# Kernel tuning notes

Hardware: AMD Instinct MI355X
Metric: run time of the kernel (lower is better)

The kernel has to match this reference:

```python
import jax, jax.numpy as jnp
import numpy as np

B, D, S, SE, H, DFF = 4, 1024, 1024, 1024, 16, 4096
DH = D // H
NUDGE = 1e-7


def norm(x):
    # x: [B, D, S]; custom layer norm: mean over (1,2), then divide by full L2 norm
    size = x.shape[1] * x.shape[2]
    mean = jnp.sum(x, axis=(1, 2)) / size
    x = x - mean[:, None, None]
    std = jnp.sqrt(jnp.sum(x * x, axis=(1, 2)))
    return x / (std[:, None, None] + NUDGE)


def mha(q_in, kv_in, Wq, Wk, Wv, Wo, causal):
    # q_in: [B, Sq, D], kv_in: [B, Sk, D]
    Bq, Sq, _ = q_in.shape
    Sk = kv_in.shape[1]
    q = (q_in @ Wq).reshape(Bq, Sq, H, DH)
    k = (kv_in @ Wk).reshape(Bq, Sk, H, DH)
    v = (kv_in @ Wv).reshape(Bq, Sk, H, DH)
    scores = jnp.einsum('bqhd,bkhd->bhqk', q, k) / jnp.sqrt(jnp.asarray(DH, q.dtype))
    if causal:
        mask = jnp.tril(jnp.ones((Sq, Sk), dtype=bool))
        scores = jnp.where(mask, scores, jnp.finfo(scores.dtype).min)
    attn = jax.nn.softmax(scores, axis=-1)
    out = jnp.einsum('bhqk,bkhd->bqhd', attn, v).reshape(Bq, Sq, D)
    return out @ Wo


def setup_inputs() -> dict:
    key = jax.random.key(0)
    ks = jax.random.split(key, 13)
    w = lambda k, sh: jax.random.normal(k, sh, dtype=jnp.float32) * 0.02
    return {
        'embedding': jax.random.normal(ks[0], (B, D, SE), dtype=jnp.float32),
        'other_inputs': jax.random.normal(ks[1], (B, D, S), dtype=jnp.float32),
        'Wq_s': w(ks[2], (D, D)), 'Wk_s': w(ks[3], (D, D)),
        'Wv_s': w(ks[4], (D, D)), 'Wo_s': w(ks[5], (D, D)),
        'Wq_c': w(ks[6], (D, D)), 'Wk_c': w(ks[7], (D, D)),
        'Wv_c': w(ks[8], (D, D)), 'Wo_c': w(ks[9], (D, D)),
        'W1': w(ks[10], (D, DFF)), 'b1': jnp.zeros((DFF,), jnp.float32),
        'W2': w(ks[11], (DFF, D)), 'b2': jnp.zeros((D,), jnp.float32),
    }


def reference(embedding, other_inputs, Wq_s, Wk_s, Wv_s, Wo_s,
              Wq_c, Wk_c, Wv_c, Wo_c, W1, b1, W2, b2):
    # tensors are [B, D, S]; attention operates on [B, S, D]
    x = other_inputs.transpose(0, 2, 1)
    sa = mha(x, x, Wq_s, Wk_s, Wv_s, Wo_s, causal=True)
    post_attention = norm(other_inputs + sa.transpose(0, 2, 1))

    pa = post_attention.transpose(0, 2, 1)
    emb = embedding.transpose(0, 2, 1)
    ca = mha(pa, emb, Wq_c, Wk_c, Wv_c, Wo_c, causal=False)
    post_embedding = norm(post_attention + ca.transpose(0, 2, 1))

    # per-token MLP (original loops over axis 2 and restacks; here fully batched)
    pe = post_embedding.transpose(0, 2, 1)  # [B, S, D]
    ff = jax.nn.relu(pe @ W1 + b1) @ W2 + b2
    return norm(post_embedding + ff.transpose(0, 2, 1))
```

## Files before the change

### kernel.cpp

```cpp
#include <hip/hip_runtime.h>
#include <cmath>

#define B_   4
#define D_   1024
#define S_   1024
#define H_   16
#define DH_  64
#define DFF_ 4096

typedef __attribute__((ext_vector_type(8))) short bf16x8;
typedef __attribute__((ext_vector_type(4))) float f32x4;

__device__ __forceinline__ unsigned short f2b(float f) {
    unsigned int u = __float_as_uint(f);
    u += 0x7fffu + ((u >> 16) & 1u);
    return (unsigned short)(u >> 16);
}

__device__ __forceinline__ void gload_lds16(const unsigned short* g, unsigned short* l) {
    __builtin_amdgcn_global_load_lds(
        (const __attribute__((address_space(1))) void*)g,
        (__attribute__((address_space(3))) void*)l, 16, 0, 0);
}

template <int BM, int BN, bool RES>
__global__ __launch_bounds__(256, 2)
void gemm_t(const unsigned short* __restrict__ A,
            const unsigned short* __restrict__ Wt,
            const float* __restrict__ bias,
            const float* __restrict__ residual,
            float* __restrict__ Cf, unsigned short* __restrict__ Cb,
            float* __restrict__ partial,
            int N, int K, int lda, int ldb, long csplit, int relu)
{
    constexpr int FM = BM / 32, FN = BN / 32;
    __shared__ unsigned short As[BM * 32];
    __shared__ unsigned short Bs[BN * 32];
    const int tid = threadIdx.x;
    const int w = tid >> 6, lane = tid & 63;
    const int quad = lane >> 4, l16 = lane & 15;
    const int m0 = blockIdx.x * BM, n0 = blockIdx.y * BN;
    const int wm = (w >> 1) * (BM / 2), wn = (w & 1) * (BN / 2);
    const int srow = lane >> 2, scol = (lane & 3) * 8;

    A  += (size_t)blockIdx.z * K;
    Wt += (size_t)blockIdx.z * K;
    if (Cf) Cf += (size_t)blockIdx.z * csplit;

    f32x4 acc[FM][FN] = {};

    for (int k0 = 0; k0 < K; k0 += 32) {
#pragma unroll
        for (int i = 0; i < BM / 64; ++i)
            gload_lds16(A + (size_t)(m0 + (w + 4 * i) * 16 + srow) * lda + k0 + scol,
                        As + (w + 4 * i) * 512);
#pragma unroll
        for (int i = 0; i < BN / 64; ++i)
            gload_lds16(Wt + (size_t)(n0 + (w + 4 * i) * 16 + srow) * ldb + k0 + scol,
                        Bs + (w + 4 * i) * 512);
        __syncthreads();

        bf16x8 af[FM], bfr[FN];
#pragma unroll
        for (int i = 0; i < FM; ++i)
            af[i] = *(const bf16x8*)&As[(wm + i * 16 + l16) * 32 + quad * 8];
#pragma unroll
        for (int j = 0; j < FN; ++j)
            bfr[j] = *(const bf16x8*)&Bs[(wn + j * 16 + l16) * 32 + quad * 8];
#pragma unroll
        for (int i = 0; i < FM; ++i)
#pragma unroll
            for (int j = 0; j < FN; ++j)
                acc[i][j] = __builtin_amdgcn_mfma_f32_16x16x32_bf16(af[i], bfr[j], acc[i][j], 0, 0, 0);
        __syncthreads();
    }

    float s = 0.f, ss = 0.f;
#pragma unroll
    for (int i = 0; i < FM; ++i) {
        const int grow = m0 + wm + i * 16 + quad * 4;
#pragma unroll
        for (int j = 0; j < FN; ++j) {
            const int gcol = n0 + wn + j * 16 + l16;
            const float bv = bias ? bias[gcol] : 0.f;
#pragma unroll
            for (int r = 0; r < 4; ++r) {
                float vv = acc[i][j][r] + bv;
                if (relu) vv = fmaxf(vv, 0.f);
                if constexpr (RES) {
                    vv += residual[(size_t)(grow + r) * N + gcol];
                    s += vv; ss += vv * vv;
                    Cf[(size_t)(grow + r) * N + gcol] = vv;
                } else {
                    if (Cf) Cf[(size_t)(grow + r) * N + gcol] = vv;
                    if (Cb) Cb[(size_t)(grow + r) * N + gcol] = f2b(vv);
                }
            }
        }
    }

    if constexpr (RES) {
        float* rs = (float*)As;
        float* rss = rs + 256;
        rs[tid] = s; rss[tid] = ss;
        __syncthreads();
        for (int off = 128; off > 0; off >>= 1) {
            if (tid < off) { rs[tid] += rs[tid + off]; rss[tid] += rss[tid + off]; }
            __syncthreads();
        }
        if (tid == 0) {
            constexpr int YPB = S_ / BM;
            const int b = blockIdx.x / YPB;
            const int chunk = (blockIdx.x % YPB) * gridDim.y + blockIdx.y;
            const int chunks = YPB * gridDim.y;
            partial[((size_t)b * chunks + chunk) * 2 + 0] = rs[0];
            partial[((size_t)b * chunks + chunk) * 2 + 1] = rss[0];
        }
    }
}

__global__ void reduce2_res(const float* __restrict__ pc, const float* __restrict__ res,
                            const float* __restrict__ bias, float* __restrict__ y,
                            float* __restrict__ partial)
{
    const size_t pcs = (size_t)4096 * 1024;
    const int b = blockIdx.y;
    const size_t base = (size_t)b * 1048576 + (size_t)blockIdx.x * 16384;
    float s = 0.f, ss = 0.f;
    for (int i = threadIdx.x; i < 4096; i += 256) {
        const size_t e = base + (size_t)i * 4;
        float4 v0 = *(const float4*)&pc[e];
        float4 v1 = *(const float4*)&pc[e + pcs];
        float4 rv = *(const float4*)&res[e];
        float4 bv = *(const float4*)&bias[e & 1023];
        float4 o;
        o.x = v0.x + v1.x + rv.x + bv.x;
        o.y = v0.y + v1.y + rv.y + bv.y;
        o.z = v0.z + v1.z + rv.z + bv.z;
        o.w = v0.w + v1.w + rv.w + bv.w;
        *(float4*)&y[e] = o;
        s += o.x + o.y + o.z + o.w;
        ss += o.x * o.x + o.y * o.y + o.z * o.z + o.w * o.w;
    }
    __shared__ float rs[256], rss[256];
    rs[threadIdx.x] = s; rss[threadIdx.x] = ss;
    __syncthreads();
    for (int off = 128; off > 0; off >>= 1) {
        if (threadIdx.x < off) {
            rs[threadIdx.x] += rs[threadIdx.x + off];
            rss[threadIdx.x] += rss[threadIdx.x + off];
        }
        __syncthreads();
    }
    if (threadIdx.x == 0) {
        partial[((size_t)b * 64 + blockIdx.x) * 2 + 0] = rs[0];
        partial[((size_t)b * 64 + blockIdx.x) * 2 + 1] = rss[0];
    }
}

__device__ __forceinline__ void stats_reduce(const float* __restrict__ partial,
                                             int b, int chunks, int tid,
                                             float* rs, float* rss,
                                             float& mean, float& inv)
{
    float s = 0.f, ss = 0.f;
    for (int i = tid; i < chunks; i += 256) {
        s  += partial[((size_t)b * chunks + i) * 2 + 0];
        ss += partial[((size_t)b * chunks + i) * 2 + 1];
    }
    rs[tid] = s; rss[tid] = ss;
    __syncthreads();
    for (int off = 128; off > 0; off >>= 1) {
        if (tid < off) { rs[tid] += rs[tid + off]; rss[tid] += rss[tid + off]; }
        __syncthreads();
    }
    const float size = (float)(D_ * S_);
    const float m = rs[0] / size;
    const float var = fmaxf(rss[0] - size * m * m, 0.f);
    mean = m;
    inv = 1.f / (sqrtf(var) + 1e-7f);
    __syncthreads();
}

__global__ void norm_apply_dual(float* __restrict__ y, unsigned short* __restrict__ yb,
                                const float* __restrict__ partial, int chunks)
{
    __shared__ float rs[256], rss[256];
    const int b = blockIdx.y;
    float mean, inv;
    stats_reduce(partial, b, chunks, threadIdx.x, rs, rss, mean, inv);

    const int perBatch = D_ * S_;
    float4* y4 = (float4*)(y + (size_t)b * perBatch);
    unsigned short* yb_ = yb + (size_t)b * perBatch;
    const int n4 = perBatch / 4;
    for (int i = blockIdx.x * blockDim.x + threadIdx.x; i < n4;
         i += gridDim.x * blockDim.x) {
        float4 v = y4[i];
        v.x = (v.x - mean) * inv; v.y = (v.y - mean) * inv;
        v.z = (v.z - mean) * inv; v.w = (v.w - mean) * inv;
        y4[i] = v;
        ushort4 hh; hh.x = f2b(v.x); hh.y = f2b(v.y); hh.z = f2b(v.z); hh.w = f2b(v.w);
        *(ushort4*)(yb_ + (size_t)i * 4) = hh;
    }
}

template <bool CAUSAL>
__global__ __launch_bounds__(256, 2)
void attn_mfma2(const unsigned short* __restrict__ q, const unsigned short* __restrict__ k,
                const unsigned short* __restrict__ vt, unsigned short* __restrict__ o,
                int qstride, int kstride)
{
    __shared__ unsigned short Ks[64][72];
    __shared__ unsigned short Vt[64][72];
    __shared__ unsigned short Ps[4][2][16][72];
    const int tid = threadIdx.x;
    const int w = tid >> 6, lane = tid & 63;
    const int quad = lane >> 4, l16 = lane & 15;
    const int h = blockIdx.y, b = blockIdx.z;
    const int qt = CAUSAL ? ((blockIdx.x + h) & 7) : blockIdx.x;
    const int q0 = qt * 128;

    const unsigned short* qA = q + (size_t)(b * S_ + q0 + w * 16 + l16) * qstride + h * DH_;
    const unsigned short* qB = qA + (size_t)64 * qstride;
    const bf16x8 qa0 = *(const bf16x8*)(qA + quad * 8);
    const bf16x8 qa1 = *(const bf16x8*)(qA + 32 + quad * 8);
    const bf16x8 qb0 = *(const bf16x8*)(qB + quad * 8);
    const bf16x8 qb1 = *(const bf16x8*)(qB + 32 + quad * 8);

    f32x4 OA[4] = {}, OB[4] = {};
    float lA[4] = {}, lB[4] = {};

    const int nblk = CAUSAL ? (2 * qt + 2) : (S_ / 64);
    for (int t = 0; t < nblk; ++t) {
        const int j0 = t * 64;
#pragma unroll
        for (int it = 0; it < 2; ++it) {
            const int id2 = tid + it * 256;
            const int row = id2 >> 3, c8 = (id2 & 7) * 8;
            *(bf16x8*)&Ks[row][c8] =
                *(const bf16x8*)(k + (size_t)(b * S_ + j0 + row) * kstride + h * DH_ + c8);
            *(bf16x8*)&Vt[row][c8] =
                *(const bf16x8*)(vt + (size_t)((b * H_ + h) * DH_ + row) * S_ + j0 + c8);
        }
        __syncthreads();

        const bool doA = !CAUSAL || (t <= 2 * qt);
        const bool diagA = CAUSAL && (t == 2 * qt);
        const bool diagB = CAUSAL && (t == 2 * qt + 1);

        f32x4 stA[4], stB[4];
#pragma unroll
        for (int n = 0; n < 4; ++n) {
            const bf16x8 kf0 = *(const bf16x8*)&Ks[n * 16 + l16][quad * 8];
            const bf16x8 kf1 = *(const bf16x8*)&Ks[n * 16 + l16][32 + quad * 8];
            if (doA) {
                f32x4 c = {};
                c = __builtin_amdgcn_mfma_f32_16x16x32_bf16(qa0, kf0, c, 0, 0, 0);
                c = __builtin_amdgcn_mfma_f32_16x16x32_bf16(qa1, kf1, c, 0, 0, 0);
                stA[n] = c;
            }
            f32x4 c = {};
            c = __builtin_amdgcn_mfma_f32_16x16x32_bf16(qb0, kf0, c, 0, 0, 0);
            c = __builtin_amdgcn_mfma_f32_16x16x32_bf16(qb1, kf1, c, 0, 0, 0);
            stB[n] = c;
        }

        if (doA) {
#pragma unroll
            for (int n = 0; n < 4; ++n)
#pragma unroll
                for (int r = 0; r < 4; ++r) {
                    float sv = stA[n][r] * 0.125f;
                    if (diagA) {
                        const int row = q0 + w * 16 + quad * 4 + r;
                        const int key = j0 + n * 16 + l16;
                        if (key > row) sv = -1e30f;
                    }
                    const float p = __expf(sv);
                    lA[r] += p;
                    Ps[w][0][quad * 4 + r][n * 16 + l16] = f2b(p);
                }
        }
#pragma unroll
        for (int n = 0; n < 4; ++n)
#pragma unroll
            for (int r = 0; r < 4; ++r) {
                float sv = stB[n][r] * 0.125f;
                if (diagB) {
                    const int row = q0 + 64 + w * 16 + quad * 4 + r;
                    const int key = j0 + n * 16 + l16;
                    if (key > row) sv = -1e30f;
                }
                const float p = __expf(sv);
                lB[r] += p;
                Ps[w][1][quad * 4 + r][n * 16 + l16] = f2b(p);
            }
        __threadfence_block();

        const bf16x8 pa0 = *(const bf16x8*)&Ps[w][0][l16][quad * 8];
        const bf16x8 pa1 = *(const bf16x8*)&Ps[w][0][l16][32 + quad * 8];
        const bf16x8 pb0 = *(const bf16x8*)&Ps[w][1][l16][quad * 8];
        const bf16x8 pb1 = *(const bf16x8*)&Ps[w][1][l16][32 + quad * 8];
#pragma unroll
        for (int n = 0; n < 4; ++n) {
            const bf16x8 vf0 = *(const bf16x8*)&Vt[n * 16 + l16][quad * 8];
            const bf16x8 vf1 = *(const bf16x8*)&Vt[n * 16 + l16][32 + quad * 8];
            if (doA) {
                OA[n] = __builtin_amdgcn_mfma_f32_16x16x32_bf16(pa0, vf0, OA[n], 0, 0, 0);
                OA[n] = __builtin_amdgcn_mfma_f32_16x16x32_bf16(pa1, vf1, OA[n], 0, 0, 0);
            }
            OB[n] = __builtin_amdgcn_mfma_f32_16x16x32_bf16(pb0, vf0, OB[n], 0, 0, 0);
            OB[n] = __builtin_amdgcn_mfma_f32_16x16x32_bf16(pb1, vf1, OB[n], 0, 0, 0);
        }
        __syncthreads();
    }

#pragma unroll
    for (int r = 0; r < 4; ++r) {
        float la = lA[r], lb = lB[r];
        la += __shfl_xor(la, 1); la += __shfl_xor(la, 2);
        la += __shfl_xor(la, 4); la += __shfl_xor(la, 8);
        lb += __shfl_xor(lb, 1); lb += __shfl_xor(lb, 2);
        lb += __shfl_xor(lb, 4); lb += __shfl_xor(lb, 8);
        const float ia = 1.f / la, ib = 1.f / lb;
        const size_t baseA = (size_t)(b * S_ + q0 + w * 16 + quad * 4 + r) * D_ + h * DH_;
        const size_t baseB = baseA + (size_t)64 * D_;
#pragma unroll
        for (int n = 0; n < 4; ++n) {
            o[baseA + n * 16 + l16] = f2b(OA[n][r] * ia);
            o[baseB + n * 16 + l16] = f2b(OB[n][r] * ib);
        }
    }
}

__global__ void transpose_v(const unsigned short* __restrict__ src,
                            unsigned short* __restrict__ dst, int istride)
{
    __shared__ unsigned short t[32][34];
    const int z = blockIdx.z, b = z >> 4, h = z & 15;
    const int s0 = blockIdx.x * 32, d0 = blockIdx.y * 32;
    const int tx = threadIdx.x, ty = threadIdx.y;
#pragma unroll
    for (int i = 0; i < 4; ++i)
        t[ty + i * 8][tx] =
            src[(size_t)(b * S_ + s0 + ty + i * 8) * istride + h * DH_ + d0 + tx];
    __syncthreads();
#pragma unroll
    for (int i = 0; i < 4; ++i)
        dst[(size_t)(z * DH_ + d0 + ty + i * 8) * S_ + s0 + tx] = t[tx][ty + i * 8];
}

struct SrcPack { const float* p[8]; };

__global__ void wtrans8(SrcPack pk, unsigned short* __restrict__ dst)
{
    __shared__ float tile[32][33];
    const int z = blockIdx.z;
    const float* src = pk.p[z];
    const int c0 = blockIdx.x * 32, r0 = blockIdx.y * 32;
    const int tx = threadIdx.x, ty = threadIdx.y;
#pragma unroll
    for (int i = 0; i < 4; ++i)
        tile[ty + i * 8][tx] = src[(size_t)(r0 + ty + i * 8) * 1024 + c0 + tx];
    __syncthreads();
#pragma unroll
    for (int i = 0; i < 4; ++i)
        dst[(size_t)z * 1048576 + (size_t)(c0 + ty + i * 8) * 1024 + r0 + tx] =
            f2b(tile[tx][ty + i * 8]);
}

__global__ void transpose_dual(const float* __restrict__ in, float* __restrict__ outf,
                               unsigned short* __restrict__ outb, int R, int C,
                               const float* __restrict__ partial, int chunks)
{
    __shared__ float tile[32][33];
    __shared__ float rs[256], rss[256];
    const int z = blockIdx.z;
    const int tx = threadIdx.x, ty = threadIdx.y;
    const int tid = ty * 32 + tx;

    float mean = 0.f, inv = 1.f;
    if (partial) {
        float s = 0.f, ss = 0.f;
        for (int i = tid; i < chunks; i += 256) {
            s  += partial[((size_t)z * chunks + i) * 2 + 0];
            ss += partial[((size_t)z * chunks + i) * 2 + 1];
        }
        rs[tid] = s; rss[tid] = ss;
        __syncthreads();
        for (int off = 128; off > 0; off >>= 1) {
            if (tid < off) { rs[tid] += rs[tid + off]; rss[tid] += rss[tid + off]; }
            __syncthreads();
        }
        const float size = (float)(D_ * S_);
        mean = rs[0] / size;
        const float var = fmaxf(rss[0] - size * mean * mean, 0.f);
        inv = 1.f / (sqrtf(var) + 1e-7f);
        __syncthreads();
    }

    const float* ip = in + (size_t)z * R * C;
    const int c0 = blockIdx.x * 32, r0 = blockIdx.y * 32;
#pragma unroll
    for (int i = 0; i < 4; ++i)
        tile[ty + i * 8][tx] = ip[(size_t)(r0 + ty + i * 8) * C + c0 + tx];
    __syncthreads();
#pragma unroll
    for (int i = 0; i < 4; ++i) {
        const float v = (tile[tx][ty + i * 8] - mean) * inv;
        const size_t oidx = (size_t)z * R * C + (size_t)(c0 + ty + i * 8) * R + r0 + tx;
        if (outf) outf[oidx] = v;
        if (outb) outb[oidx] = f2b(v);
    }
}

extern "C" void kernel_launch(void* const* d_in, const int* in_sizes, int n_in,
                              void* d_out, int out_size, void* d_ws, size_t ws_size,
                              hipStream_t stream)
{
    const float* embedding = (const float*)d_in[0];
    const float* other     = (const float*)d_in[1];
    const float* W1 = (const float*)d_in[10];
    const float* b1 = (const float*)d_in[11];
    const float* W2 = (const float*)d_in[12];
    const float* b2 = (const float*)d_in[13];
    float* out = (float*)d_out;

    char* wsb = (char*)d_ws;
    const size_t MB = 1u << 20;
    float* f0 = (float*)(wsb + 0 * MB);
    float* f2 = (float*)(wsb + 16 * MB);
    unsigned short* wts  = (unsigned short*)(wsb + 32 * MB);
    unsigned short* wqkv = wts;
    unsigned short* wo_s = wts + 3 * 1048576;
    unsigned short* wq_c = wts + 4 * 1048576;
    unsigned short* wkv_c= wts + 5 * 1048576;
    unsigned short* wo_c = wts + 7 * 1048576;
    unsigned short* w1t  = wts + 8 * 1048576;
    unsigned short* w2t  = wts + 12 * 1048576;
    unsigned short* actA = (unsigned short*)(wsb + 64 * MB);
    unsigned short* actB = (unsigned short*)(wsb + 72 * MB);
    unsigned short* actC = (unsigned short*)(wsb + 80 * MB);
    unsigned short* actC2 = actC + 4 * 1048576;
    float* pc      = (float*)(wsb + 112 * MB);
    float* partial = (float*)(wsb + 176 * MB);

    const dim3 blkT(32, 8), blk256(256);
    const dim3 gT(32, 32, B_);
    const dim3 gAttn(S_ / 128, H_, B_);
    const dim3 gVt(32, 2, B_ * H_);
    const dim3 gApply(64, B_);

    SrcPack pk;
    pk.p[0] = (const float*)d_in[2]; pk.p[1] = (const float*)d_in[3];
    pk.p[2] = (const float*)d_in[4]; pk.p[3] = (const float*)d_in[5];
    pk.p[4] = (const float*)d_in[6]; pk.p[5] = (const float*)d_in[7];
    pk.p[6] = (const float*)d_in[8]; pk.p[7] = (const float*)d_in[9];
    hipLaunchKernelGGL(wtrans8, dim3(32, 32, 8), blkT, 0, stream, pk, wts);
    hipLaunchKernelGGL(transpose_dual, dim3(128, 32, 1), blkT, 0, stream, W1, nullptr, w1t, 1024, 4096, nullptr, 0);
    hipLaunchKernelGGL(transpose_dual, dim3(32, 128, 1), blkT, 0, stream, W2, nullptr, w2t, 4096, 1024, nullptr, 0);

    hipLaunchKernelGGL(transpose_dual, gT, blkT, 0, stream, other, f0, actA, D_, S_, nullptr, 0);

    hipLaunchKernelGGL((gemm_t<128, 128, false>), dim3(32, 24), blk256, 0, stream,
                       actA, wqkv, nullptr, nullptr, nullptr, actC, nullptr,
                       3072, 1024, 1024, 1024, 0L, 0);
    hipLaunchKernelGGL(transpose_v, gVt, blkT, 0, stream, actC + 2048, actA, 3072);
    hipLaunchKernelGGL(attn_mfma2<true>, gAttn, blk256, 0, stream,
                       actC, actC + 1024, actA, actB, 3072, 3072);
    hipLaunchKernelGGL((gemm_t<64, 128, true>), dim3(64, 8), blk256, 0, stream,
                       actB, wo_s, nullptr, f0, f2, nullptr, partial,
                       1024, 1024, 1024, 1024, 0L, 0);
    hipLaunchKernelGGL(norm_apply_dual, gApply, blk256, 0, stream, f2, actA, partial, 128);

    hipLaunchKernelGGL(transpose_dual, gT, blkT, 0, stream, embedding, nullptr, actB, D_, S_, nullptr, 0);
    hipLaunchKernelGGL((gemm_t<64, 128, false>), dim3(64, 8), blk256, 0, stream,
                       actA, wq_c, nullptr, nullptr, nullptr, actC, nullptr,
                       1024, 1024, 1024, 1024, 0L, 0);
    hipLaunchKernelGGL((gemm_t<128, 128, false>), dim3(32, 16), blk256, 0, stream,
                       actB, wkv_c, nullptr, nullptr, nullptr, actC2, nullptr,
                       2048, 1024, 1024, 1024, 0L, 0);
    hipLaunchKernelGGL(transpose_v, gVt, blkT, 0, stream, actC2 + 1024, actB, 2048);
    hipLaunchKernelGGL(attn_mfma2<false>, gAttn, blk256, 0, stream,
                       actC, actC2, actB, actA, 1024, 2048);
    hipLaunchKernelGGL((gemm_t<64, 128, true>), dim3(64, 8), blk256, 0, stream,
                       actA, wo_c, nullptr, f2, f0, nullptr, partial,
                       1024, 1024, 1024, 1024, 0L, 0);
    hipLaunchKernelGGL(norm_apply_dual, gApply, blk256, 0, stream, f0, actA, partial, 128);

    hipLaunchKernelGGL((gemm_t<128, 128, false>), dim3(32, 32), blk256, 0, stream,
                       actA, w1t, b1, nullptr, nullptr, actC, nullptr,
                       DFF_, 1024, 1024, 1024, 0L, 1);
    hipLaunchKernelGGL((gemm_t<128, 128, false>), dim3(32, 8, 2), blk256, 0, stream,
                       actC, w2t, nullptr, nullptr, pc, nullptr, nullptr,
                       1024, 2048, 4096, 4096, (long)4096 * 1024, 0);
    hipLaunchKernelGGL(reduce2_res, gApply, blk256, 0, stream, pc, f0, b2, f2, partial);
    hipLaunchKernelGGL(transpose_dual, gT, blkT, 0, stream, f2, out, nullptr, S_, D_, partial, 64);

    (void)in_sizes; (void)n_in; (void)out_size; (void)ws_size;
}
```

Before: 535.0 us.

## Double GEMM K-tile with XOR-swizzled LDS and merge transpose launches

The GEMM now stages 64-wide K tiles per iteration instead of 32, using an XOR swizzle on the LDS column index to avoid bank conflicts on the MFMA fragment reads. This halves the number of barrier pairs per K sweep at the cost of doubling shared memory, which may affect occupancy. All weight transposes are merged into one launch, and the two input transposes into another, cutting launch count. The attention output moves to a separate buffer so the embedding transpose can run early.

```diff
diff --git a/kernel.cpp b/kernel.cpp
--- a/kernel.cpp
+++ b/kernel.cpp
@@ -34,14 +34,15 @@
             int N, int K, int lda, int ldb, long csplit, int relu)
 {
     constexpr int FM = BM / 32, FN = BN / 32;
-    __shared__ unsigned short As[BM * 32];
-    __shared__ unsigned short Bs[BN * 32];
+    __shared__ unsigned short As[BM * 64];
+    __shared__ unsigned short Bs[BN * 64];
     const int tid = threadIdx.x;
     const int w = tid >> 6, lane = tid & 63;
     const int quad = lane >> 4, l16 = lane & 15;
     const int m0 = blockIdx.x * BM, n0 = blockIdx.y * BN;
     const int wm = (w >> 1) * (BM / 2), wn = (w & 1) * (BN / 2);
-    const int srow = lane >> 2, scol = (lane & 3) * 8;
+    const int srow = lane >> 3;
+    const int scol = ((lane & 7) ^ srow) * 8;
 
     A  += (size_t)blockIdx.z * K;
     Wt += (size_t)blockIdx.z * K;
@@ -49,29 +50,40 @@
 
     f32x4 acc[FM][FN] = {};
 
-    for (int k0 = 0; k0 < K; k0 += 32) {
-#pragma unroll
-        for (int i = 0; i < BM / 64; ++i)
-            gload_lds16(A + (size_t)(m0 + (w + 4 * i) * 16 + srow) * lda + k0 + scol,
-                        As + (w + 4 * i) * 512);
-#pragma unroll
-        for (int i = 0; i < BN / 64; ++i)
-            gload_lds16(Wt + (size_t)(n0 + (w + 4 * i) * 16 + srow) * ldb + k0 + scol,
-                        Bs + (w + 4 * i) * 512);
-        __syncthreads();
-
-        bf16x8 af[FM], bfr[FN];
-#pragma unroll
-        for (int i = 0; i < FM; ++i)
-            af[i] = *(const bf16x8*)&As[(wm + i * 16 + l16) * 32 + quad * 8];
-#pragma unroll
-        for (int j = 0; j < FN; ++j)
-            bfr[j] = *(const bf16x8*)&Bs[(wn + j * 16 + l16) * 32 + quad * 8];
-#pragma unroll
-        for (int i = 0; i < FM; ++i)
-#pragma unroll
-            for (int j = 0; j < FN; ++j)
-                acc[i][j] = __builtin_amdgcn_mfma_f32_16x16x32_bf16(af[i], bfr[j], acc[i][j], 0, 0, 0);
+    for (int k0 = 0; k0 < K; k0 += 64) {
+#pragma unroll
+        for (int i = 0; i < BM / 32; ++i) {
+            const int inst = w + 4 * i;
+            gload_lds16(A + (size_t)(m0 + inst * 8 + srow) * lda + k0 + scol,
+                        As + inst * 512);
+        }
+#pragma unroll
+        for (int i = 0; i < BN / 32; ++i) {
+            const int inst = w + 4 * i;
+            gload_lds16(Wt + (size_t)(n0 + inst * 8 + srow) * ldb + k0 + scol,
+                        Bs + inst * 512);
+        }
+        __syncthreads();
+
+#pragma unroll
+        for (int kk = 0; kk < 2; ++kk) {
+            bf16x8 af[FM], bfr[FN];
+#pragma unroll
+            for (int i = 0; i < FM; ++i) {
+                const int r = wm + i * 16 + l16;
+                af[i] = *(const bf16x8*)&As[r * 64 + (((kk * 4 + quad) ^ (r & 7)) * 8)];
+            }
+#pragma unroll
+            for (int j = 0; j < FN; ++j) {
+                const int r = wn + j * 16 + l16;
+                bfr[j] = *(const bf16x8*)&Bs[r * 64 + (((kk * 4 + quad) ^ (r & 7)) * 8)];
+            }
+#pragma unroll
+            for (int i = 0; i < FM; ++i)
+#pragma unroll
+                for (int j = 0; j < FN; ++j)
+                    acc[i][j] = __builtin_amdgcn_mfma_f32_16x16x32_bf16(af[i], bfr[j], acc[i][j], 0, 0, 0);
+        }
         __syncthreads();
     }
 
@@ -351,28 +363,51 @@
         dst[(size_t)(z * DH_ + d0 + ty + i * 8) * S_ + s0 + tx] = t[tx][ty + i * 8];
 }
 
-struct SrcPack { const float* p[8]; };
-
-__global__ void wtrans8(SrcPack pk, unsigned short* __restrict__ dst)
+struct WJob { const float* src; int sld; long doff; int dld; };
+struct WJobs { WJob j[16]; };
+
+__global__ void wtrans_all(WJobs js, unsigned short* __restrict__ dst)
+{
+    __shared__ float tile[32][33];
+    const WJob J = js.j[blockIdx.z];
+    const int c0 = blockIdx.x * 32, r0 = blockIdx.y * 32;
+    const int tx = threadIdx.x, ty = threadIdx.y;
+#pragma unroll
+    for (int i = 0; i < 4; ++i)
+        tile[ty + i * 8][tx] = J.src[(size_t)(r0 + ty + i * 8) * J.sld + c0 + tx];
+    __syncthreads();
+#pragma unroll
+    for (int i = 0; i < 4; ++i)
+        dst[J.doff + (size_t)(c0 + ty + i * 8) * J.dld + r0 + tx] =
+            f2b(tile[tx][ty + i * 8]);
+}
+
+__global__ void transpose_in(const float* __restrict__ other, const float* __restrict__ emb,
+                             float* __restrict__ f0, unsigned short* __restrict__ xb,
+                             unsigned short* __restrict__ eb)
 {
     __shared__ float tile[32][33];
     const int z = blockIdx.z;
-    const float* src = pk.p[z];
+    const int b = z & 3;
+    const bool isEmb = z >= 4;
+    const float* ip = (isEmb ? emb : other) + (size_t)b * 1048576;
     const int c0 = blockIdx.x * 32, r0 = blockIdx.y * 32;
     const int tx = threadIdx.x, ty = threadIdx.y;
 #pragma unroll
     for (int i = 0; i < 4; ++i)
-        tile[ty + i * 8][tx] = src[(size_t)(r0 + ty + i * 8) * 1024 + c0 + tx];
-    __syncthreads();
-#pragma unroll
-    for (int i = 0; i < 4; ++i)
-        dst[(size_t)z * 1048576 + (size_t)(c0 + ty + i * 8) * 1024 + r0 + tx] =
-            f2b(tile[tx][ty + i * 8]);
-}
-
-__global__ void transpose_dual(const float* __restrict__ in, float* __restrict__ outf,
-                               unsigned short* __restrict__ outb, int R, int C,
-                               const float* __restrict__ partial, int chunks)
+        tile[ty + i * 8][tx] = ip[(size_t)(r0 + ty + i * 8) * 1024 + c0 + tx];
+    __syncthreads();
+#pragma unroll
+    for (int i = 0; i < 4; ++i) {
+        const float v = tile[tx][ty + i * 8];
+        const size_t oidx = (size_t)b * 1048576 + (size_t)(c0 + ty + i * 8) * 1024 + r0 + tx;
+        if (isEmb) eb[oidx] = f2b(v);
+        else { f0[oidx] = v; xb[oidx] = f2b(v); }
+    }
+}
+
+__global__ void transpose_out(const float* __restrict__ in, float* __restrict__ outf,
+                              const float* __restrict__ partial, int chunks)
 {
     __shared__ float tile[32][33];
     __shared__ float rs[256], rss[256];
@@ -380,38 +415,19 @@
     const int tx = threadIdx.x, ty = threadIdx.y;
     const int tid = ty * 32 + tx;
 
-    float mean = 0.f, inv = 1.f;
-    if (partial) {
-        float s = 0.f, ss = 0.f;
-        for (int i = tid; i < chunks; i += 256) {
-            s  += partial[((size_t)z * chunks + i) * 2 + 0];
-            ss += partial[((size_t)z * chunks + i) * 2 + 1];
-        }
-        rs[tid] = s; rss[tid] = ss;
-        __syncthreads();
-        for (int off = 128; off > 0; off >>= 1) {
-            if (tid < off) { rs[tid] += rs[tid + off]; rss[tid] += rss[tid + off]; }
-            __syncthreads();
-        }
-        const float size = (float)(D_ * S_);
-        mean = rs[0] / size;
-        const float var = fmaxf(rss[0] - size * mean * mean, 0.f);
-        inv = 1.f / (sqrtf(var) + 1e-7f);
-        __syncthreads();
-    }
-
-    const float* ip = in + (size_t)z * R * C;
+    float mean, inv;
+    stats_reduce(partial, z, chunks, tid, rs, rss, mean, inv);
+
+    const float* ip = in + (size_t)z * 1048576;
     const int c0 = blockIdx.x * 32, r0 = blockIdx.y * 32;
 #pragma unroll
     for (int i = 0; i < 4; ++i)
-        tile[ty + i * 8][tx] = ip[(size_t)(r0 + ty + i * 8) * C + c0 + tx];
+        tile[ty + i * 8][tx] = ip[(size_t)(r0 + ty + i * 8) * 1024 + c0 + tx];
     __syncthreads();
 #pragma unroll
     for (int i = 0; i < 4; ++i) {
         const float v = (tile[tx][ty + i * 8] - mean) * inv;
-        const size_t oidx = (size_t)z * R * C + (size_t)(c0 + ty + i * 8) * R + r0 + tx;
-        if (outf) outf[oidx] = v;
-        if (outb) outb[oidx] = f2b(v);
+        outf[(size_t)z * 1048576 + (size_t)(c0 + ty + i * 8) * 1024 + r0 + tx] = v;
     }
 }
 
@@ -443,38 +459,38 @@
     unsigned short* actB = (unsigned short*)(wsb + 72 * MB);
     unsigned short* actC = (unsigned short*)(wsb + 80 * MB);
     unsigned short* actC2 = actC + 4 * 1048576;
+    unsigned short* aout  = actC + 12 * 1048576;
     float* pc      = (float*)(wsb + 112 * MB);
     float* partial = (float*)(wsb + 176 * MB);
 
     const dim3 blkT(32, 8), blk256(256);
-    const dim3 gT(32, 32, B_);
     const dim3 gAttn(S_ / 128, H_, B_);
     const dim3 gVt(32, 2, B_ * H_);
     const dim3 gApply(64, B_);
 
-    SrcPack pk;
-    pk.p[0] = (const float*)d_in[2]; pk.p[1] = (const float*)d_in[3];
-    pk.p[2] = (const float*)d_in[4]; pk.p[3] = (const float*)d_in[5];
-    pk.p[4] = (const float*)d_in[6]; pk.p[5] = (const float*)d_in[7];
-    pk.p[6] = (const float*)d_in[8]; pk.p[7] = (const float*)d_in[9];
-    hipLaunchKernelGGL(wtrans8, dim3(32, 32, 8), blkT, 0, stream, pk, wts);
-    hipLaunchKernelGGL(transpose_dual, dim3(128, 32, 1), blkT, 0, stream, W1, nullptr, w1t, 1024, 4096, nullptr, 0);
-    hipLaunchKernelGGL(transpose_dual, dim3(32, 128, 1), blkT, 0, stream, W2, nullptr, w2t, 4096, 1024, nullptr, 0);
-
-    hipLaunchKernelGGL(transpose_dual, gT, blkT, 0, stream, other, f0, actA, D_, S_, nullptr, 0);
+    WJobs js;
+    for (int z = 0; z < 8; ++z)
+        js.j[z] = { (const float*)d_in[2 + z], 1024, (long)z * 1048576, 1024 };
+    for (int q = 0; q < 4; ++q)
+        js.j[8 + q] = { W1 + (size_t)q * 1024, 4096, (long)(8 + q) * 1048576, 1024 };
+    for (int q = 0; q < 4; ++q)
+        js.j[12 + q] = { W2 + (size_t)q * 1048576, 1024, 12L * 1048576 + q * 1024, 4096 };
+    hipLaunchKernelGGL(wtrans_all, dim3(32, 32, 16), blkT, 0, stream, js, wts);
+
+    hipLaunchKernelGGL(transpose_in, dim3(32, 32, 8), blkT, 0, stream,
+                       other, embedding, f0, actA, actB);
 
     hipLaunchKernelGGL((gemm_t<128, 128, false>), dim3(32, 24), blk256, 0, stream,
                        actA, wqkv, nullptr, nullptr, nullptr, actC, nullptr,
                        3072, 1024, 1024, 1024, 0L, 0);
     hipLaunchKernelGGL(transpose_v, gVt, blkT, 0, stream, actC + 2048, actA, 3072);
     hipLaunchKernelGGL(attn_mfma2<true>, gAttn, blk256, 0, stream,
-                       actC, actC + 1024, actA, actB, 3072, 3072);
+                       actC, actC + 1024, actA, aout, 3072, 3072);
     hipLaunchKernelGGL((gemm_t<64, 128, true>), dim3(64, 8), blk256, 0, stream,
-                       actB, wo_s, nullptr, f0, f2, nullptr, partial,
+                       aout, wo_s, nullptr, f0, f2, nullptr, partial,
                        1024, 1024, 1024, 1024, 0L, 0);
     hipLaunchKernelGGL(norm_apply_dual, gApply, blk256, 0, stream, f2, actA, partial, 128);
 
-    hipLaunchKernelGGL(transpose_dual, gT, blkT, 0, stream, embedding, nullptr, actB, D_, S_, nullptr, 0);
     hipLaunchKernelGGL((gemm_t<64, 128, false>), dim3(64, 8), blk256, 0, stream,
                        actA, wq_c, nullptr, nullptr, nullptr, actC, nullptr,
                        1024, 1024, 1024, 1024, 0L, 0);
@@ -483,9 +499,9 @@
                        2048, 1024, 1024, 1024, 0L, 0);
     hipLaunchKernelGGL(transpose_v, gVt, blkT, 0, stream, actC2 + 1024, actB, 2048);
     hipLaunchKernelGGL(attn_mfma2<false>, gAttn, blk256, 0, stream,
-                       actC, actC2, actB, actA, 1024, 2048);
+                       actC, actC2, actB, aout, 1024, 2048);
     hipLaunchKernelGGL((gemm_t<64, 128, true>), dim3(64, 8), blk256, 0, stream,
-                       actA, wo_c, nullptr, f2, f0, nullptr, partial,
+                       aout, wo_c, nullptr, f2, f0, nullptr, partial,
                        1024, 1024, 1024, 1024, 0L, 0);
     hipLaunchKernelGGL(norm_apply_dual, gApply, blk256, 0, stream, f0, actA, partial, 128);
 
@@ -496,7 +512,7 @@
                        actC, w2t, nullptr, nullptr, pc, nullptr, nullptr,
                        1024, 2048, 4096, 4096, (long)4096 * 1024, 0);
     hipLaunchKernelGGL(reduce2_res, gApply, blk256, 0, stream, pc, f0, b2, f2, partial);
-    hipLaunchKernelGGL(transpose_dual, gT, blkT, 0, stream, f2, out, nullptr, S_, D_, partial, 64);
+    hipLaunchKernelGGL(transpose_out, dim3(32, 32, B_), blkT, 0, stream, f2, out, partial, 64);
 
     (void)in_sizes; (void)n_in; (void)out_size; (void)ws_size;
 }
```

After: 514.2 us. 1.04x faster.
